# Optimization experiments

Hardware: AMD Instinct MI355X
Metric: run time of the kernel (lower is better)

## Reference

```python
import jax, jax.numpy as jnp
import numpy as np

EPS = 1e-12  # tf.math.l2_normalize epsilon

def _l2norm(x):
    # normalize over last axis, matching K.l2_normalize semantics
    sq = jnp.sum(x * x, axis=-1, keepdims=True)
    return x * jax.lax.rsqrt(jnp.maximum(sq, EPS))

def setup_inputs() -> dict:
    key = jax.random.key(0)
    k1, k2, k3 = jax.random.split(key, 3)
    B, L, D, P = 16, 256, 256, 20
    sent1 = jax.random.normal(k1, (B, L, D), dtype=jnp.float32)
    sent2 = jax.random.normal(k2, (B, L, D), dtype=jnp.float32)
    # glorot_uniform for shape (P, D)
    limit = np.sqrt(6.0 / (P + D)).astype(np.float32)
    kernel = jax.random.uniform(k3, (P, D), minval=-limit, maxval=limit, dtype=jnp.float32)
    return {"sent1": sent1, "sent2": sent2, "kernel": kernel}

def reference(sent1, sent2, kernel):
    # sent1: [B,L1,D], sent2: [B,L2,D], kernel: [P,D]
    v1 = _l2norm(sent1[:, :, None, :] * kernel)  # [B,L1,P,D]
    v2 = _l2norm(sent2[:, :, None, :] * kernel)  # [B,L2,P,D]
    # per-perspective cosine similarity matrix: [B,L1,L2,P]
    cos = jnp.einsum('blpd,bmpd->blmp', v1, v2)
    # max over the other sentence's positions (L2) -> [B,L1,P]
    return jnp.max(cos, axis=2)
```

## Files before the change

kernel.cpp:

```cpp
#include <hip/hip_runtime.h>
#include <hip/hip_bf16.h>


#define B_DIM 16
#define L_DIM 256
#define D_DIM 256
#define P_DIM 20
#define EPS 1e-12f
#define LDP 264

typedef __attribute__((ext_vector_type(8))) __bf16 bf16x8;
typedef __attribute__((ext_vector_type(4))) float f32x4;

__device__ __forceinline__ unsigned short f2bf(float x) {
  unsigned int u = __float_as_uint(x);
  u += 0x7fffu + ((u >> 16) & 1u);
  return (unsigned short)(u >> 16);
}

__global__ __launch_bounds__(256)
void prep2(const float* __restrict__ s1, const float* __restrict__ s2,
           const float* __restrict__ kg,
           float* __restrict__ rn1, float* __restrict__ rn2,
           unsigned short* __restrict__ s1bf, unsigned short* __restrict__ s2bf) {
  __shared__ __align__(16) unsigned short QA[32 * LDP];
  __shared__ __align__(16) unsigned short QB[32 * LDP];
  const int tid = threadIdx.x, lane = tid & 63, wave = tid >> 6;
  const int lr = lane & 15, q = lane >> 4;
  const int sent = blockIdx.x & 1, t = blockIdx.x >> 1;
  const int r0 = t * 32, b = r0 >> 8;
  const float* src = sent ? s2 : s1;
  unsigned short* sbf = sent ? s2bf : s1bf;
  float* rn = sent ? rn2 : rn1;

  #pragma unroll
  for (int i = 0; i < 8; ++i) {
    const int row = i * 4 + wave;
    float4 sv = *(const float4*)(src + (size_t)(r0 + row) * D_DIM + lane * 4);
    unsigned int c0 = ((unsigned int)f2bf(sv.y) << 16) | f2bf(sv.x);
    unsigned int c1 = ((unsigned int)f2bf(sv.w) << 16) | f2bf(sv.z);
    *(uint2*)&sbf[(size_t)(r0 + row) * D_DIM + lane * 4] = make_uint2(c0, c1);
    unsigned int q0 = ((unsigned int)f2bf(sv.y * sv.y) << 16) | f2bf(sv.x * sv.x);
    unsigned int q1 = ((unsigned int)f2bf(sv.w * sv.w) << 16) | f2bf(sv.z * sv.z);
    *(uint2*)&QA[row * LDP + lane * 4] = make_uint2(q0, q1);
  }
  #pragma unroll
  for (int j = 0; j < 5; ++j) {
    const int row = wave * 5 + j;
    float4 kv = *(const float4*)(kg + row * D_DIM + lane * 4);
    unsigned int c0 = ((unsigned int)f2bf(kv.y * kv.y) << 16) | f2bf(kv.x * kv.x);
    unsigned int c1 = ((unsigned int)f2bf(kv.w * kv.w) << 16) | f2bf(kv.z * kv.z);
    *(uint2*)&QB[row * LDP + lane * 4] = make_uint2(c0, c1);
  }
  __syncthreads();

  const int mt = wave & 1, nt = wave >> 1;
  f32x4 acc = {0.f, 0.f, 0.f, 0.f};
  #pragma unroll
  for (int ks = 0; ks < 8; ++ks) {
    const int cc = ks * 4 + q;
    bf16x8 a  = *(const bf16x8*)&QA[(mt * 16 + lr) * LDP + cc * 8];
    bf16x8 bb = *(const bf16x8*)&QB[(nt * 16 + lr) * LDP + cc * 8];
    acc = __builtin_amdgcn_mfma_f32_16x16x32_bf16(a, bb, acc, 0, 0, 0);
  }
  const int p = nt * 16 + lr;
  if (p < P_DIM) {
    #pragma unroll
    for (int r = 0; r < 4; ++r) {
      const int l = (r0 & 255) + mt * 16 + q * 4 + r;
      rn[((size_t)b * P_DIM + p) * L_DIM + l] = rsqrtf(fmaxf(acc[r], EPS));
    }
  }
}

__global__ __launch_bounds__(512, 1)
void mpm_main(const unsigned short* __restrict__ s1bf,
              const unsigned short* __restrict__ s2bf,
              const float* __restrict__ kg, const float* __restrict__ rn1,
              const float* __restrict__ rn2, float* __restrict__ outg) {
  __shared__ __align__(16) unsigned short X2[256 * 256];
  __shared__ __align__(16) unsigned short X1[64 * 256];
  float* WoutF = (float*)X1;

  const int tid = threadIdx.x, lane = tid & 63, wave = tid >> 6;
  const int lr = lane & 15, q = lane >> 4;
  const int bid = blockIdx.x;
  const int pgi = bid & 3, lt = (bid >> 2) & 3, b = bid >> 4;
  const int l0 = lt * 64;

  {
    const unsigned short* s2b = s2bf + (size_t)b * L_DIM * D_DIM;
    #pragma unroll
    for (int j = 0; j < 16; ++j) {
      int g = j * 512 + tid;
      int r = g >> 5, pr = g & 31;
      int c = pr ^ (r & 31);
      __builtin_amdgcn_global_load_lds(
          (const __attribute__((address_space(1))) void*)(s2b + r * 256 + c * 8),
          (__attribute__((address_space(3))) void*)(X2 + (size_t)g * 8), 16, 0, 0);
    }
  }

  uint2 s1r[8];
  {
    const unsigned short* s1b = s1bf + ((size_t)b * L_DIM + l0) * D_DIM;
    #pragma unroll
    for (int i = 0; i < 8; ++i)
      s1r[i] = *(const uint2*)(s1b + (size_t)(i * 8 + wave) * D_DIM + lane * 4);
  }

  const int mrow0 = wave * 32 + lr,  mrow1 = wave * 32 + 16 + lr;
  const int mkey0 = mrow0 & 31,      mkey1 = mrow1 & 31;

  #pragma unroll 1
  for (int pp = 0; pp < 5; ++pp) {
    const int p = pgi * 5 + pp;
    __syncthreads();

    {
      float4 kv = *(const float4*)(kg + p * D_DIM + lane * 4);
      const float k0 = kv.x * kv.x, k1 = kv.y * kv.y, k2 = kv.z * kv.z, k3 = kv.w * kv.w;
      const float* rn1b = rn1 + ((size_t)b * P_DIM + p) * L_DIM + l0;
      #pragma unroll
      for (int i = 0; i < 8; ++i) {
        const int row = i * 8 + wave;
        const float rv = rn1b[row];
        float x0 = __uint_as_float(s1r[i].x << 16)          * k0 * rv;
        float x1 = __uint_as_float(s1r[i].x & 0xffff0000u)  * k1 * rv;
        float x2 = __uint_as_float(s1r[i].y << 16)          * k2 * rv;
        float x3 = __uint_as_float(s1r[i].y & 0xffff0000u)  * k3 * rv;
        unsigned int c0 = ((unsigned int)f2bf(x1) << 16) | f2bf(x0);
        unsigned int c1 = ((unsigned int)f2bf(x3) << 16) | f2bf(x2);
        *(uint2*)&X1[row * 256 + (((lane >> 1) ^ (row & 31)) << 3) + ((lane & 1) << 2)] =
            make_uint2(c0, c1);
      }
    }
    __syncthreads();

    f32x4 acc[2][4];
    #pragma unroll
    for (int mi = 0; mi < 2; ++mi)
      #pragma unroll
      for (int li = 0; li < 4; ++li) acc[mi][li] = (f32x4){0.f, 0.f, 0.f, 0.f};

    #pragma unroll
    for (int ks = 0; ks < 8; ++ks) {
      const int cc = ks * 4 + q;
      bf16x8 a0 = *(const bf16x8*)&X2[mrow0 * 256 + ((cc ^ mkey0) << 3)];
      bf16x8 a1 = *(const bf16x8*)&X2[mrow1 * 256 + ((cc ^ mkey1) << 3)];
      bf16x8 bb[4];
      #pragma unroll
      for (int li = 0; li < 4; ++li) {
        const int l = li * 16 + lr;
        bb[li] = *(const bf16x8*)&X1[l * 256 + ((cc ^ (l & 31)) << 3)];
      }
      #pragma unroll
      for (int li = 0; li < 4; ++li) {
        acc[0][li] = __builtin_amdgcn_mfma_f32_16x16x32_bf16(a0, bb[li], acc[0][li], 0, 0, 0);
        acc[1][li] = __builtin_amdgcn_mfma_f32_16x16x32_bf16(a1, bb[li], acc[1][li], 0, 0, 0);
      }
    }

    float4 r20, r21;
    {
      const float* rn2b = rn2 + ((size_t)b * P_DIM + p) * L_DIM + wave * 32;
      r20 = *(const float4*)(rn2b + q * 4);
      r21 = *(const float4*)(rn2b + 16 + q * 4);
    }
    float v[4];
    #pragma unroll
    for (int li = 0; li < 4; ++li) {
      float t = -3.4e38f;
      t = fmaxf(t, fmaxf(acc[0][li][0] * r20.x, acc[1][li][0] * r21.x));
      t = fmaxf(t, fmaxf(acc[0][li][1] * r20.y, acc[1][li][1] * r21.y));
      t = fmaxf(t, fmaxf(acc[0][li][2] * r20.z, acc[1][li][2] * r21.z));
      t = fmaxf(t, fmaxf(acc[0][li][3] * r20.w, acc[1][li][3] * r21.w));
      t = fmaxf(t, __shfl_xor(t, 16));
      t = fmaxf(t, __shfl_xor(t, 32));
      v[li] = t;
    }

    __syncthreads();
    if (q == 0) {
      #pragma unroll
      for (int li = 0; li < 4; ++li) WoutF[wave * 64 + li * 16 + lr] = v[li];
    }
    __syncthreads();
    if (tid < 64) {
      float o = WoutF[tid];
      #pragma unroll
      for (int w = 1; w < 8; ++w) o = fmaxf(o, WoutF[w * 64 + tid]);
      outg[((size_t)b * L_DIM + (l0 + tid)) * P_DIM + p] = o;
    }
  }
}

extern "C" void kernel_launch(void* const* d_in, const int* in_sizes, int n_in,
                              void* d_out, int out_size, void* d_ws, size_t ws_size,
                              hipStream_t stream) {
  const float* s1 = (const float*)d_in[0];
  const float* s2 = (const float*)d_in[1];
  const float* kg = (const float*)d_in[2];
  float* out = (float*)d_out;

  float* rn1 = (float*)d_ws;
  float* rn2 = rn1 + (size_t)B_DIM * P_DIM * L_DIM;
  unsigned short* s2bf = (unsigned short*)(rn2 + (size_t)B_DIM * P_DIM * L_DIM);
  unsigned short* s1bf = s2bf + (size_t)B_DIM * L_DIM * D_DIM;

  prep2<<<dim3(256), dim3(256), 0, stream>>>(s1, s2, kg, rn1, rn2, s1bf, s2bf);
  mpm_main<<<dim3(256), dim3(512), 0, stream>>>(s1bf, s2bf, kg, rn1, rn2, out);
}
```

Measured before the change: 82.60 us.

## Keep sent2 MFMA operands in registers and halve the sentence-1 tile per block

The main kernel no longer stages the whole bf16 sent2 tile (128 KB) in LDS. Each wave now loads its 64 rows of sent2 directly into registers as MFMA A operands. Blocks shrink to 256 threads over 32 sentence-1 rows, which doubles the grid and allows two blocks per CU. A barrier at the top of the loop is removed, and the cross-wave max reduction now spans 4 waves. This cuts LDS traffic and LDS capacity pressure. In exchange it uses heavy register pressure (128 VGPRs for operands alone) and doubles how often each sent2 slice is re-read from global/L2.

Result: slower. 85.45 us (+3.5%).

```diff
diff --git a/kernel.cpp b/kernel.cpp
--- a/kernel.cpp
+++ b/kernel.cpp
@@ -73,31 +73,29 @@
   }
 }
 
-__global__ __launch_bounds__(512, 1)
+__global__ __launch_bounds__(256, 2)
 void mpm_main(const unsigned short* __restrict__ s1bf,
               const unsigned short* __restrict__ s2bf,
               const float* __restrict__ kg, const float* __restrict__ rn1,
               const float* __restrict__ rn2, float* __restrict__ outg) {
-  __shared__ __align__(16) unsigned short X2[256 * 256];
-  __shared__ __align__(16) unsigned short X1[64 * 256];
-  float* WoutF = (float*)X1;
+  __shared__ __align__(16) unsigned short X1[32 * 256];
+  __shared__ float Wout[4 * 32];
 
   const int tid = threadIdx.x, lane = tid & 63, wave = tid >> 6;
   const int lr = lane & 15, q = lane >> 4;
   const int bid = blockIdx.x;
-  const int pgi = bid & 3, lt = (bid >> 2) & 3, b = bid >> 4;
-  const int l0 = lt * 64;
-
+  const int pgi = bid & 3, lt = (bid >> 2) & 7, b = bid >> 5;
+  const int l0 = lt * 32;
+
+  bf16x8 areg[4][8];
   {
     const unsigned short* s2b = s2bf + (size_t)b * L_DIM * D_DIM;
     #pragma unroll
-    for (int j = 0; j < 16; ++j) {
-      int g = j * 512 + tid;
-      int r = g >> 5, pr = g & 31;
-      int c = pr ^ (r & 31);
-      __builtin_amdgcn_global_load_lds(
-          (const __attribute__((address_space(1))) void*)(s2b + r * 256 + c * 8),
-          (__attribute__((address_space(3))) void*)(X2 + (size_t)g * 8), 16, 0, 0);
+    for (int mi = 0; mi < 4; ++mi) {
+      const unsigned short* rp = s2b + (size_t)(wave * 64 + mi * 16 + lr) * D_DIM + q * 8;
+      #pragma unroll
+      for (int ks = 0; ks < 8; ++ks)
+        areg[mi][ks] = *(const bf16x8*)(rp + ks * 32);
     }
   }
 
@@ -106,16 +104,12 @@
     const unsigned short* s1b = s1bf + ((size_t)b * L_DIM + l0) * D_DIM;
     #pragma unroll
     for (int i = 0; i < 8; ++i)
-      s1r[i] = *(const uint2*)(s1b + (size_t)(i * 8 + wave) * D_DIM + lane * 4);
-  }
-
-  const int mrow0 = wave * 32 + lr,  mrow1 = wave * 32 + 16 + lr;
-  const int mkey0 = mrow0 & 31,      mkey1 = mrow1 & 31;
+      s1r[i] = *(const uint2*)(s1b + (size_t)(i * 4 + wave) * D_DIM + lane * 4);
+  }
 
   #pragma unroll 1
   for (int pp = 0; pp < 5; ++pp) {
     const int p = pgi * 5 + pp;
-    __syncthreads();
 
     {
       float4 kv = *(const float4*)(kg + p * D_DIM + lane * 4);
@@ -123,73 +117,68 @@
       const float* rn1b = rn1 + ((size_t)b * P_DIM + p) * L_DIM + l0;
       #pragma unroll
       for (int i = 0; i < 8; ++i) {
-        const int row = i * 8 + wave;
+        const int row = i * 4 + wave;
         const float rv = rn1b[row];
-        float x0 = __uint_as_float(s1r[i].x << 16)          * k0 * rv;
-        float x1 = __uint_as_float(s1r[i].x & 0xffff0000u)  * k1 * rv;
-        float x2 = __uint_as_float(s1r[i].y << 16)          * k2 * rv;
-        float x3 = __uint_as_float(s1r[i].y & 0xffff0000u)  * k3 * rv;
+        float x0 = __uint_as_float(s1r[i].x << 16)         * k0 * rv;
+        float x1 = __uint_as_float(s1r[i].x & 0xffff0000u) * k1 * rv;
+        float x2 = __uint_as_float(s1r[i].y << 16)         * k2 * rv;
+        float x3 = __uint_as_float(s1r[i].y & 0xffff0000u) * k3 * rv;
         unsigned int c0 = ((unsigned int)f2bf(x1) << 16) | f2bf(x0);
         unsigned int c1 = ((unsigned int)f2bf(x3) << 16) | f2bf(x2);
-        *(uint2*)&X1[row * 256 + (((lane >> 1) ^ (row & 31)) << 3) + ((lane & 1) << 2)] =
+        *(uint2*)&X1[row * 256 + (((lane >> 1) ^ row) << 3) + ((lane & 1) << 2)] =
             make_uint2(c0, c1);
       }
     }
     __syncthreads();
 
-    f32x4 acc[2][4];
-    #pragma unroll
-    for (int mi = 0; mi < 2; ++mi)
-      #pragma unroll
-      for (int li = 0; li < 4; ++li) acc[mi][li] = (f32x4){0.f, 0.f, 0.f, 0.f};
-
+    f32x4 acc[4][2];
+    #pragma unroll
+    for (int mi = 0; mi < 4; ++mi) {
+      acc[mi][0] = (f32x4){0.f, 0.f, 0.f, 0.f};
+      acc[mi][1] = (f32x4){0.f, 0.f, 0.f, 0.f};
+    }
     #pragma unroll
     for (int ks = 0; ks < 8; ++ks) {
       const int cc = ks * 4 + q;
-      bf16x8 a0 = *(const bf16x8*)&X2[mrow0 * 256 + ((cc ^ mkey0) << 3)];
-      bf16x8 a1 = *(const bf16x8*)&X2[mrow1 * 256 + ((cc ^ mkey1) << 3)];
-      bf16x8 bb[4];
-      #pragma unroll
-      for (int li = 0; li < 4; ++li) {
-        const int l = li * 16 + lr;
-        bb[li] = *(const bf16x8*)&X1[l * 256 + ((cc ^ (l & 31)) << 3)];
+      bf16x8 b0 = *(const bf16x8*)&X1[(lr)      * 256 + ((cc ^ lr) << 3)];
+      bf16x8 b1 = *(const bf16x8*)&X1[(16 + lr) * 256 + ((cc ^ (16 + lr)) << 3)];
+      #pragma unroll
+      for (int mi = 0; mi < 4; ++mi) {
+        acc[mi][0] = __builtin_amdgcn_mfma_f32_16x16x32_bf16(areg[mi][ks], b0, acc[mi][0], 0, 0, 0);
+        acc[mi][1] = __builtin_amdgcn_mfma_f32_16x16x32_bf16(areg[mi][ks], b1, acc[mi][1], 0, 0, 0);
       }
-      #pragma unroll
-      for (int li = 0; li < 4; ++li) {
-        acc[0][li] = __builtin_amdgcn_mfma_f32_16x16x32_bf16(a0, bb[li], acc[0][li], 0, 0, 0);
-        acc[1][li] = __builtin_amdgcn_mfma_f32_16x16x32_bf16(a1, bb[li], acc[1][li], 0, 0, 0);
+    }
+
+    float4 r2[4];
+    {
+      const float* rn2b = rn2 + ((size_t)b * P_DIM + p) * L_DIM + wave * 64;
+      #pragma unroll
+      for (int mi = 0; mi < 4; ++mi)
+        r2[mi] = *(const float4*)(rn2b + mi * 16 + q * 4);
+    }
+    float v[2];
+    #pragma unroll
+    for (int li = 0; li < 2; ++li) {
+      float t = -3.4e38f;
+      #pragma unroll
+      for (int mi = 0; mi < 4; ++mi) {
+        t = fmaxf(t, acc[mi][li][0] * r2[mi].x);
+        t = fmaxf(t, acc[mi][li][1] * r2[mi].y);
+        t = fmaxf(t, acc[mi][li][2] * r2[mi].z);
+        t = fmaxf(t, acc[mi][li][3] * r2[mi].w);
       }
-    }
-
-    float4 r20, r21;
-    {
-      const float* rn2b = rn2 + ((size_t)b * P_DIM + p) * L_DIM + wave * 32;
-      r20 = *(const float4*)(rn2b + q * 4);
-      r21 = *(const float4*)(rn2b + 16 + q * 4);
-    }
-    float v[4];
-    #pragma unroll
-    for (int li = 0; li < 4; ++li) {
-      float t = -3.4e38f;
-      t = fmaxf(t, fmaxf(acc[0][li][0] * r20.x, acc[1][li][0] * r21.x));
-      t = fmaxf(t, fmaxf(acc[0][li][1] * r20.y, acc[1][li][1] * r21.y));
-      t = fmaxf(t, fmaxf(acc[0][li][2] * r20.z, acc[1][li][2] * r21.z));
-      t = fmaxf(t, fmaxf(acc[0][li][3] * r20.w, acc[1][li][3] * r21.w));
       t = fmaxf(t, __shfl_xor(t, 16));
       t = fmaxf(t, __shfl_xor(t, 32));
       v[li] = t;
     }
-
+    if (q == 0) {
+      Wout[wave * 32 + lr]      = v[0];
+      Wout[wave * 32 + 16 + lr] = v[1];
+    }
     __syncthreads();
-    if (q == 0) {
-      #pragma unroll
-      for (int li = 0; li < 4; ++li) WoutF[wave * 64 + li * 16 + lr] = v[li];
-    }
-    __syncthreads();
-    if (tid < 64) {
-      float o = WoutF[tid];
-      #pragma unroll
-      for (int w = 1; w < 8; ++w) o = fmaxf(o, WoutF[w * 64 + tid]);
+    if (tid < 32) {
+      float o = fmaxf(fmaxf(Wout[tid], Wout[32 + tid]),
+                      fmaxf(Wout[64 + tid], Wout[96 + tid]));
       outg[((size_t)b * L_DIM + (l0 + tid)) * P_DIM + p] = o;
     }
   }
@@ -209,5 +198,5 @@
   unsigned short* s1bf = s2bf + (size_t)B_DIM * L_DIM * D_DIM;
 
   prep2<<<dim3(256), dim3(256), 0, stream>>>(s1, s2, kg, rn1, rn2, s1bf, s2bf);
-  mpm_main<<<dim3(256), dim3(512), 0, stream>>>(s1bf, s2bf, kg, rn1, rn2, out);
-}
+  mpm_main<<<dim3(512), dim3(256), 0, stream>>>(s1bf, s2bf, kg, rn1, rn2, out);
+}
```
